# Optimization experiments

Measured on AMD Instinct MI355X. Metric: run time of the kernel, lower is better.

Reference implementation:

```python
import jax, jax.numpy as jnp
import numpy as np

B, C, H, W = 8, 64, 64, 64
PROJ = 8


def setup_inputs() -> dict:
    key = jax.random.key(0)
    ks = jax.random.split(key, 8)
    inp = {
        "query_x": jax.random.normal(ks[0], (B, C, H, W), dtype=jnp.float32),
        "ref_x": jax.random.normal(ks[1], (B, C, H, W), dtype=jnp.float32),
        # 1x1 conv weights stored as [out_ch, in_ch] (kernel_size=1)
        "wq": jax.random.normal(ks[2], (PROJ, C), dtype=jnp.float32) * 0.05,
        "bq": jnp.zeros((PROJ,), dtype=jnp.float32),
        "wk": jax.random.normal(ks[3], (PROJ, C), dtype=jnp.float32) * 0.05,
        "bk": jnp.zeros((PROJ,), dtype=jnp.float32),
        "wv": jax.random.normal(ks[4], (C, C), dtype=jnp.float32) * 0.05,
        "bv": jnp.zeros((C,), dtype=jnp.float32),
    }
    return inp


def reference(query_x, ref_x, wq, bq, wk, bk, wv, bv):
    b, c, h, w = ref_x.shape
    n = h * w
    # 1x1 conv projections, flattened to [B, ch, HW]
    q = (jnp.einsum("oc,bchw->bohw", wq, query_x) + bq[None, :, None, None]).reshape(b, PROJ, n)
    k = (jnp.einsum("oc,bchw->bohw", wk, ref_x) + bk[None, :, None, None]).reshape(b, PROJ, n)
    v = (jnp.einsum("oc,bchw->bohw", wv, ref_x) + bv[None, :, None, None]).reshape(b, c, n)
    # energy[b, j(ref), i(query)] = sum_p k[b,p,j] * q[b,p,i]  (unscaled)
    energy = jnp.einsum("bpj,bpi->bji", k, q)
    attention = jax.nn.softmax(energy, axis=-1)
    # z = bmm(v, attention^T): z[b,c,j] = sum_i v[b,c,i] * attention[b,j,i]
    z = jnp.einsum("bci,bji->bcj", v, attention).reshape(b, c, h, w)
    return query_x + z
```

## Files before the change

kernel.cpp:

```cpp
#include <hip/hip_runtime.h>
#include <hip/hip_bf16.h>

#define B_ 8
#define C_ 64
#define N_ 4096
#define ITERS 16

typedef __attribute__((ext_vector_type(4))) short bf16x4;
typedef __attribute__((ext_vector_type(8))) short bf16x8;
typedef __attribute__((ext_vector_type(4))) float f32x4;

static __device__ inline ushort f2bf(float x) {
    union { float f; unsigned u; } c; c.f = x;
    return (ushort)((c.u + 0x7FFFu + ((c.u >> 16) & 1u)) >> 16);
}
static __device__ inline short f2bfs(float x) {
    __hip_bfloat16 h = __float2bfloat16(x);
    return *reinterpret_cast<short*>(&h);
}
static __device__ inline int4 pack8(const ushort* s) {
    int4 r;
    r.x = (int)(s[0] | ((unsigned)s[1] << 16));
    r.y = (int)(s[2] | ((unsigned)s[3] << 16));
    r.z = (int)(s[4] | ((unsigned)s[5] << 16));
    r.w = (int)(s[6] | ((unsigned)s[7] << 16));
    return r;
}
static __device__ inline float exp2fast(float x) {
#if __has_builtin(__builtin_amdgcn_exp2f)
    return __builtin_amdgcn_exp2f(x);
#else
    return exp2f(x);
#endif
}

#if __has_builtin(__builtin_amdgcn_mfma_f32_16x16x16bf16_1k)
static __device__ inline f32x4 mfma16(bf16x4 a, bf16x4 b, f32x4 c) {
    return __builtin_amdgcn_mfma_f32_16x16x16bf16_1k(a, b, c, 0, 0, 0);
}
#else
static __device__ inline f32x4 mfma16(bf16x4 a, bf16x4 b, f32x4 c) {
    bf16x8 a8 = (bf16x8){a[0], a[1], a[2], a[3], 0, 0, 0, 0};
    bf16x8 b8 = (bf16x8){b[0], b[1], b[2], b[3], 0, 0, 0, 0};
    return __builtin_amdgcn_mfma_f32_16x16x32_bf16(a8, b8, c, 0, 0, 0);
}
#endif

static __device__ inline void gload16(const void* g, void* l) {
#if __has_builtin(__builtin_amdgcn_global_load_lds)
    __builtin_amdgcn_global_load_lds(
        (const __attribute__((address_space(1))) void*)g,
        (__attribute__((address_space(3))) void*)l, 16, 0, 0);
#else
    const int lane = threadIdx.x & 63;
    *(int4*)((char*)l + lane * 16) = *(const int4*)((const char*)g + lane * 16);
#endif
}

__global__ __launch_bounds__(256) void proj_kernel(
    const float* __restrict__ qx, const float* __restrict__ rx,
    const float* __restrict__ wq, const float* __restrict__ bq,
    const float* __restrict__ wk, const float* __restrict__ bk,
    const float* __restrict__ wv, const float* __restrict__ bv,
    ushort* __restrict__ qb, ushort* __restrict__ kb, ushort* __restrict__ vt2)
{
    const int og  = blockIdx.y;
    const int gid = blockIdx.x * 256 + threadIdx.x;
    const int b   = gid >> 12;
    const int i   = gid & (N_ - 1);

    if (og <= 1) {
        const float* xp = (og == 0 ? qx : rx) + (size_t)b * C_ * N_ + i;
        const float* wp = (og == 0 ? wq : wk);
        const float* bp = (og == 0 ? bq : bk);
        const float scale = (og == 0) ? 1.0f : 1.44269504088896340736f;
        float a[8];
#pragma unroll
        for (int p = 0; p < 8; ++p) a[p] = bp[p];
        for (int c = 0; c < C_; ++c) {
            const float x = xp[(size_t)c * N_];
#pragma unroll
            for (int p = 0; p < 8; ++p) a[p] = fmaf(wp[p * C_ + c], x, a[p]);
        }
        ushort u8[8];
#pragma unroll
        for (int p = 0; p < 8; ++p) u8[p] = f2bf(a[p] * scale);
        ushort* dst = (og == 0 ? qb : kb) + (size_t)gid * 8;
        *(int4*)dst = pack8(u8);
    } else {
        const int o0 = (og - 2) * 16;
        const float* xp = rx + (size_t)b * C_ * N_ + i;
        float a[16];
#pragma unroll
        for (int p = 0; p < 16; ++p) a[p] = bv[o0 + p];
        for (int c = 0; c < C_; ++c) {
            const float x = xp[(size_t)c * N_];
#pragma unroll
            for (int p = 0; p < 16; ++p)
                a[p] = fmaf(wv[(o0 + p) * C_ + c], x, a[p]);
        }
        const int t  = i >> 5;
        const int lo = i & 7;
        const int hi = (i >> 3) & 3;
        ushort* tb = vt2 + ((size_t)(b * 128 + t)) * 2048;
#pragma unroll
        for (int p = 0; p < 16; ++p) {
            const int c = o0 + p;
            tb[c * 32 + (((hi ^ ((c >> 1) & 3))) << 3) + lo] = f2bf(a[p]);
        }
    }
}

__global__ __launch_bounds__(512, 4) void attn_kernel(
    const ushort* __restrict__ qb, const ushort* __restrict__ kb,
    const ushort* __restrict__ vt2, const float* __restrict__ qx,
    float* __restrict__ out)
{
    __shared__ __align__(16) char smem[65536];
    float* o_lds    = (float*)smem;
    float* lsum_lds = (float*)(smem + 2 * 64 * 68 * 4);

    const int tid  = threadIdx.x;
    const int ig   = tid >> 6;
    const int lane = tid & 63;
    const int cc   = lane & 15;
    const int g    = lane >> 4;
    const int b    = blockIdx.y;
    const int j0   = blockIdx.x * 64;

    bf16x4 bk[4];
#pragma unroll
    for (int jb = 0; jb < 4; ++jb) bk[jb] = (bf16x4){0, 0, 0, 0};
    if (g < 2) {
#pragma unroll
        for (int jb = 0; jb < 4; ++jb)
            bk[jb] = *(const bf16x4*)(kb + ((size_t)b * N_ + j0 + jb * 16 + cc) * 8 + g * 4);
    }

    const int qperm = 8 * (cc >> 2) + (cc & 3);
    const ushort* qptr = qb + ((size_t)b * N_ + (size_t)ig * (N_ / 8) + qperm) * 8 + g * 4;

    const char* vsl = (const char*)vt2 + ((size_t)(b * 128 + ig * 16)) * 4096 + lane * 16;
    char* lds0 = smem + ig * 8192;

    f32x4 acc[4][4];
#pragma unroll
    for (int jb = 0; jb < 4; ++jb)
#pragma unroll
        for (int ct = 0; ct < 4; ++ct) acc[jb][ct] = (f32x4){0.f, 0.f, 0.f, 0.f};
    float ls[4] = {0.f, 0.f, 0.f, 0.f};
    const f32x4 zero4 = (f32x4){0.f, 0.f, 0.f, 0.f};

    {
        const char* s = vsl;
        char* d = lds0;
        gload16(s, d);
        gload16(s + 1024, d + 1024);
        gload16(s + 2048, d + 2048);
        gload16(s + 3072, d + 3072);
    }
    bf16x4 aq0 = *(const bf16x4*)(qptr);
    bf16x4 aq1 = *(const bf16x4*)(qptr + 32);

    const int rb = cc * 32 + ((g ^ ((cc >> 1) & 3)) << 3);

    int cur = 0;
#pragma unroll 1
    for (int it = 0; it < ITERS; ++it) {
        asm volatile("s_waitcnt vmcnt(0)" ::: "memory");
        __builtin_amdgcn_sched_barrier(0);

        const ushort* vtile = (const ushort*)(lds0 + cur * 4096);
        bf16x8 av0 = *(const bf16x8*)(vtile + rb);
        bf16x8 av1 = *(const bf16x8*)(vtile + rb + 512);
        bf16x8 av2 = *(const bf16x8*)(vtile + rb + 1024);
        bf16x8 av3 = *(const bf16x8*)(vtile + rb + 1536);

        const int nxt = (it + 1) & (ITERS - 1);
        {
            const char* s = vsl + (size_t)nxt * 4096;
            char* d = lds0 + (cur ^ 1) * 4096;
            gload16(s, d);
            gload16(s + 1024, d + 1024);
            gload16(s + 2048, d + 2048);
            gload16(s + 3072, d + 3072);
        }

#pragma unroll
        for (int jb = 0; jb < 4; ++jb) {
            f32x4 e0 = mfma16(aq0, bk[jb], zero4);
            f32x4 e1 = mfma16(aq1, bk[jb], zero4);
            float p[8];
#pragma unroll
            for (int r = 0; r < 4; ++r) {
                p[r]     = exp2fast(e0[r]);
                p[4 + r] = exp2fast(e1[r]);
            }
            bf16x8 pb;
#pragma unroll
            for (int e = 0; e < 8; ++e) pb[e] = f2bfs(p[e]);
            ls[jb] += ((p[0] + p[1]) + (p[2] + p[3])) +
                      ((p[4] + p[5]) + (p[6] + p[7]));
            acc[jb][0] = __builtin_amdgcn_mfma_f32_16x16x32_bf16(av0, pb, acc[jb][0], 0, 0, 0);
            acc[jb][1] = __builtin_amdgcn_mfma_f32_16x16x32_bf16(av1, pb, acc[jb][1], 0, 0, 0);
            acc[jb][2] = __builtin_amdgcn_mfma_f32_16x16x32_bf16(av2, pb, acc[jb][2], 0, 0, 0);
            acc[jb][3] = __builtin_amdgcn_mfma_f32_16x16x32_bf16(av3, pb, acc[jb][3], 0, 0, 0);
        }

        {
            const ushort* qp = qptr + (size_t)nxt * 256;
            aq0 = *(const bf16x4*)(qp);
            aq1 = *(const bf16x4*)(qp + 32);
        }
        cur ^= 1;
    }

#pragma unroll
    for (int jb = 0; jb < 4; ++jb) {
        ls[jb] += __shfl_xor(ls[jb], 16, 64);
        ls[jb] += __shfl_xor(ls[jb], 32, 64);
    }

    __syncthreads();
    {
        const int phme = ig >> 1;
        float* od = o_lds + (ig & 1) * (64 * 68);
        float* ld = lsum_lds + (ig & 1) * 64;
#pragma unroll 1
        for (int ph = 0; ph < 4; ++ph) {
            if (phme == ph) {
                if (ph == 0) {
#pragma unroll
                    for (int jb = 0; jb < 4; ++jb)
#pragma unroll
                        for (int ct = 0; ct < 4; ++ct)
#pragma unroll
                            for (int r = 0; r < 4; ++r)
                                od[(ct * 16 + 4 * g + r) * 68 + jb * 16 + cc] = acc[jb][ct][r];
                    if (g == 0) {
#pragma unroll
                        for (int jb = 0; jb < 4; ++jb) ld[jb * 16 + cc] = ls[jb];
                    }
                } else {
#pragma unroll
                    for (int jb = 0; jb < 4; ++jb)
#pragma unroll
                        for (int ct = 0; ct < 4; ++ct)
#pragma unroll
                            for (int r = 0; r < 4; ++r)
                                od[(ct * 16 + 4 * g + r) * 68 + jb * 16 + cc] += acc[jb][ct][r];
                    if (g == 0) {
#pragma unroll
                        for (int jb = 0; jb < 4; ++jb) ld[jb * 16 + cc] += ls[jb];
                    }
                }
            }
            __syncthreads();
        }
    }

    const int ec = tid >> 3;
    const int ej = (tid & 7) * 8;
    const float* xp = qx  + ((size_t)b * C_ + ec) * N_ + j0 + ej;
    float*       op = out + ((size_t)b * C_ + ec) * N_ + j0 + ej;
    float4 x0 = *(const float4*)xp;
    float4 x1 = *(const float4*)(xp + 4);
    float rr[8];
#pragma unroll
    for (int t = 0; t < 8; ++t) {
        const float num = o_lds[ec * 68 + ej + t] + o_lds[64 * 68 + ec * 68 + ej + t];
        const float den = lsum_lds[ej + t] + lsum_lds[64 + ej + t];
        rr[t] = num / den;
    }
    float4 r0 = make_float4(x0.x + rr[0], x0.y + rr[1], x0.z + rr[2], x0.w + rr[3]);
    float4 r1 = make_float4(x1.x + rr[4], x1.y + rr[5], x1.z + rr[6], x1.w + rr[7]);
    *(float4*)op       = r0;
    *(float4*)(op + 4) = r1;
}

extern "C" void kernel_launch(void* const* d_in, const int* in_sizes, int n_in,
                              void* d_out, int out_size, void* d_ws, size_t ws_size,
                              hipStream_t stream) {
    const float* qx = (const float*)d_in[0];
    const float* rx = (const float*)d_in[1];
    const float* wq = (const float*)d_in[2];
    const float* bq = (const float*)d_in[3];
    const float* wk = (const float*)d_in[4];
    const float* bk = (const float*)d_in[5];
    const float* wv = (const float*)d_in[6];
    const float* bv = (const float*)d_in[7];
    float* out = (float*)d_out;

    ushort* qb  = (ushort*)d_ws;
    ushort* kb  = qb + (size_t)B_ * N_ * 8;
    ushort* vt2 = kb + (size_t)B_ * N_ * 8;

    proj_kernel<<<dim3((B_ * N_) / 256, 6), 256, 0, stream>>>(
        qx, rx, wq, bq, wk, bk, wv, bv, qb, kb, vt2);

    attn_kernel<<<dim3(N_ / 64, B_), 512, 0, stream>>>(qb, kb, vt2, qx, out);
}
```

Measured before the change: 52.57 us.

## Fuse K/V projection reads, double-register Q prefetch, packed bf16 convert, swap grid order

The projection kernel drops from six to three output groups: one group computes K together with the first 32 V channels so ref_x is read fewer times, and each V group now covers 32 channels. The attention loop is unrolled by two with separate Q registers so Q loads are prefetched two iterations ahead, and it waits with vmcnt(2) instead of draining all loads. The exp results are converted with packed float2-to-bf16 intrinsics and summed as float2 vectors. The attention grid is transposed so batch is the fast block index. Larger per-thread accumulators (40 floats) raise register pressure in the projection kernel and halve its grid size.

```diff
diff --git a/kernel.cpp b/kernel.cpp
--- a/kernel.cpp
+++ b/kernel.cpp
@@ -8,23 +8,12 @@
 
 typedef __attribute__((ext_vector_type(4))) short bf16x4;
 typedef __attribute__((ext_vector_type(8))) short bf16x8;
+typedef __attribute__((ext_vector_type(2))) float f32x2;
 typedef __attribute__((ext_vector_type(4))) float f32x4;
 
 static __device__ inline ushort f2bf(float x) {
     union { float f; unsigned u; } c; c.f = x;
     return (ushort)((c.u + 0x7FFFu + ((c.u >> 16) & 1u)) >> 16);
-}
-static __device__ inline short f2bfs(float x) {
-    __hip_bfloat16 h = __float2bfloat16(x);
-    return *reinterpret_cast<short*>(&h);
-}
-static __device__ inline int4 pack8(const ushort* s) {
-    int4 r;
-    r.x = (int)(s[0] | ((unsigned)s[1] << 16));
-    r.y = (int)(s[2] | ((unsigned)s[3] << 16));
-    r.z = (int)(s[4] | ((unsigned)s[5] << 16));
-    r.w = (int)(s[6] | ((unsigned)s[7] << 16));
-    return r;
 }
 static __device__ inline float exp2fast(float x) {
 #if __has_builtin(__builtin_amdgcn_exp2f)
@@ -45,6 +34,9 @@
     return __builtin_amdgcn_mfma_f32_16x16x32_bf16(a8, b8, c, 0, 0, 0);
 }
 #endif
+static __device__ inline f32x4 mfma32(bf16x8 a, bf16x8 b, f32x4 c) {
+    return __builtin_amdgcn_mfma_f32_16x16x32_bf16(a, b, c, 0, 0, 0);
+}
 
 static __device__ inline void gload16(const void* g, void* l) {
 #if __has_builtin(__builtin_amdgcn_global_load_lds)
@@ -69,44 +61,72 @@
     const int b   = gid >> 12;
     const int i   = gid & (N_ - 1);
 
-    if (og <= 1) {
-        const float* xp = (og == 0 ? qx : rx) + (size_t)b * C_ * N_ + i;
-        const float* wp = (og == 0 ? wq : wk);
-        const float* bp = (og == 0 ? bq : bk);
-        const float scale = (og == 0) ? 1.0f : 1.44269504088896340736f;
+    const int t  = i >> 5;
+    const int lo = i & 7;
+    const int hi = (i >> 3) & 3;
+    ushort* tb = vt2 + ((size_t)(b * 128 + t)) * 2048;
+
+    if (og == 0) {
+        const float* xp = qx + (size_t)b * C_ * N_ + i;
         float a[8];
 #pragma unroll
-        for (int p = 0; p < 8; ++p) a[p] = bp[p];
+        for (int p = 0; p < 8; ++p) a[p] = bq[p];
         for (int c = 0; c < C_; ++c) {
             const float x = xp[(size_t)c * N_];
 #pragma unroll
-            for (int p = 0; p < 8; ++p) a[p] = fmaf(wp[p * C_ + c], x, a[p]);
+            for (int p = 0; p < 8; ++p) a[p] = fmaf(wq[p * C_ + c], x, a[p]);
         }
         ushort u8[8];
 #pragma unroll
-        for (int p = 0; p < 8; ++p) u8[p] = f2bf(a[p] * scale);
-        ushort* dst = (og == 0 ? qb : kb) + (size_t)gid * 8;
-        *(int4*)dst = pack8(u8);
-    } else {
-        const int o0 = (og - 2) * 16;
+        for (int p = 0; p < 8; ++p) u8[p] = f2bf(a[p]);
+        int4 r;
+        r.x = (int)(u8[0] | ((unsigned)u8[1] << 16));
+        r.y = (int)(u8[2] | ((unsigned)u8[3] << 16));
+        r.z = (int)(u8[4] | ((unsigned)u8[5] << 16));
+        r.w = (int)(u8[6] | ((unsigned)u8[7] << 16));
+        *(int4*)(qb + (size_t)gid * 8) = r;
+    } else if (og == 1) {
         const float* xp = rx + (size_t)b * C_ * N_ + i;
-        float a[16];
-#pragma unroll
-        for (int p = 0; p < 16; ++p) a[p] = bv[o0 + p];
+        float ak[8], av[32];
+#pragma unroll
+        for (int p = 0; p < 8; ++p) ak[p] = bk[p];
+#pragma unroll
+        for (int p = 0; p < 32; ++p) av[p] = bv[p];
         for (int c = 0; c < C_; ++c) {
             const float x = xp[(size_t)c * N_];
 #pragma unroll
-            for (int p = 0; p < 16; ++p)
-                a[p] = fmaf(wv[(o0 + p) * C_ + c], x, a[p]);
-        }
-        const int t  = i >> 5;
-        const int lo = i & 7;
-        const int hi = (i >> 3) & 3;
-        ushort* tb = vt2 + ((size_t)(b * 128 + t)) * 2048;
-#pragma unroll
-        for (int p = 0; p < 16; ++p) {
-            const int c = o0 + p;
-            tb[c * 32 + (((hi ^ ((c >> 1) & 3))) << 3) + lo] = f2bf(a[p]);
+            for (int p = 0; p < 8; ++p) ak[p] = fmaf(wk[p * C_ + c], x, ak[p]);
+#pragma unroll
+            for (int p = 0; p < 32; ++p) av[p] = fmaf(wv[p * C_ + c], x, av[p]);
+        }
+        const float s = 1.44269504088896340736f;
+        ushort u8[8];
+#pragma unroll
+        for (int p = 0; p < 8; ++p) u8[p] = f2bf(ak[p] * s);
+        int4 r;
+        r.x = (int)(u8[0] | ((unsigned)u8[1] << 16));
+        r.y = (int)(u8[2] | ((unsigned)u8[3] << 16));
+        r.z = (int)(u8[4] | ((unsigned)u8[5] << 16));
+        r.w = (int)(u8[6] | ((unsigned)u8[7] << 16));
+        *(int4*)(kb + (size_t)gid * 8) = r;
+#pragma unroll
+        for (int p = 0; p < 32; ++p)
+            tb[p * 32 + ((hi ^ ((p >> 1) & 3)) << 3) + lo] = f2bf(av[p]);
+    } else {
+        const float* xp = rx + (size_t)b * C_ * N_ + i;
+        float av[32];
+#pragma unroll
+        for (int p = 0; p < 32; ++p) av[p] = bv[32 + p];
+        for (int c = 0; c < C_; ++c) {
+            const float x = xp[(size_t)c * N_];
+#pragma unroll
+            for (int p = 0; p < 32; ++p)
+                av[p] = fmaf(wv[(32 + p) * C_ + c], x, av[p]);
+        }
+#pragma unroll
+        for (int p = 0; p < 32; ++p) {
+            const int c = 32 + p;
+            tb[c * 32 + ((hi ^ ((c >> 1) & 3)) << 3) + lo] = f2bf(av[p]);
         }
     }
 }
@@ -125,8 +145,8 @@
     const int lane = tid & 63;
     const int cc   = lane & 15;
     const int g    = lane >> 4;
-    const int b    = blockIdx.y;
-    const int j0   = blockIdx.x * 64;
+    const int b    = blockIdx.x;
+    const int j0   = blockIdx.y * 64;
 
     bf16x4 bk[4];
 #pragma unroll
@@ -148,75 +168,84 @@
     for (int jb = 0; jb < 4; ++jb)
 #pragma unroll
         for (int ct = 0; ct < 4; ++ct) acc[jb][ct] = (f32x4){0.f, 0.f, 0.f, 0.f};
-    float ls[4] = {0.f, 0.f, 0.f, 0.f};
+    f32x2 ls2[4];
+#pragma unroll
+    for (int jb = 0; jb < 4; ++jb) ls2[jb] = (f32x2){0.f, 0.f};
     const f32x4 zero4 = (f32x4){0.f, 0.f, 0.f, 0.f};
 
-    {
-        const char* s = vsl;
-        char* d = lds0;
-        gload16(s, d);
-        gload16(s + 1024, d + 1024);
-        gload16(s + 2048, d + 2048);
-        gload16(s + 3072, d + 3072);
-    }
-    bf16x4 aq0 = *(const bf16x4*)(qptr);
-    bf16x4 aq1 = *(const bf16x4*)(qptr + 32);
-
     const int rb = cc * 32 + ((g ^ ((cc >> 1) & 3)) << 3);
 
-    int cur = 0;
+    bf16x4 qa0 = *(const bf16x4*)(qptr);
+    bf16x4 qa1 = *(const bf16x4*)(qptr + 32);
+    gload16(vsl, lds0);
+    gload16(vsl + 1024, lds0 + 1024);
+    gload16(vsl + 2048, lds0 + 2048);
+    gload16(vsl + 3072, lds0 + 3072);
+    bf16x4 qb0 = *(const bf16x4*)(qptr + 256);
+    bf16x4 qb1 = *(const bf16x4*)(qptr + 256 + 32);
+    asm volatile("s_waitcnt vmcnt(0)" ::: "memory");
+    __builtin_amdgcn_sched_barrier(0);
+
+#define HALF_ITER(Q0, Q1, RBOFF, WBOFF, IT)                                    \
+    {                                                                          \
+        asm volatile("s_waitcnt vmcnt(2)" ::: "memory");                       \
+        __builtin_amdgcn_sched_barrier(0);                                     \
+        const ushort* vtile = (const ushort*)(lds0 + (RBOFF));                 \
+        bf16x8 av0 = *(const bf16x8*)(vtile + rb);                             \
+        bf16x8 av1 = *(const bf16x8*)(vtile + rb + 512);                       \
+        bf16x8 av2 = *(const bf16x8*)(vtile + rb + 1024);                      \
+        bf16x8 av3 = *(const bf16x8*)(vtile + rb + 1536);                      \
+        {                                                                      \
+            const int nxt = ((IT) + 1) & (ITERS - 1);                          \
+            const char* s = vsl + (size_t)nxt * 4096;                          \
+            char* dd = lds0 + (WBOFF);                                         \
+            gload16(s, dd);                                                    \
+            gload16(s + 1024, dd + 1024);                                      \
+            gload16(s + 2048, dd + 2048);                                      \
+            gload16(s + 3072, dd + 3072);                                      \
+        }                                                                      \
+        __builtin_amdgcn_sched_barrier(0);                                     \
+        _Pragma("unroll")                                                      \
+        for (int jb = 0; jb < 4; ++jb) {                                       \
+            f32x4 e0 = mfma16(Q0, bk[jb], zero4);                              \
+            f32x4 e1 = mfma16(Q1, bk[jb], zero4);                              \
+            float p0 = exp2fast(e0[0]), p1 = exp2fast(e0[1]);                  \
+            float p2 = exp2fast(e0[2]), p3 = exp2fast(e0[3]);                  \
+            float p4 = exp2fast(e1[0]), p5 = exp2fast(e1[1]);                  \
+            float p6 = exp2fast(e1[2]), p7 = exp2fast(e1[3]);                  \
+            union { bf16x8 v; __hip_bfloat162 h[4]; } pu;                      \
+            pu.h[0] = __float22bfloat162_rn(make_float2(p0, p1));              \
+            pu.h[1] = __float22bfloat162_rn(make_float2(p2, p3));              \
+            pu.h[2] = __float22bfloat162_rn(make_float2(p4, p5));              \
+            pu.h[3] = __float22bfloat162_rn(make_float2(p6, p7));              \
+            f32x2 sA = (f32x2){p0, p1} + (f32x2){p2, p3};                      \
+            f32x2 sB = (f32x2){p4, p5} + (f32x2){p6, p7};                      \
+            ls2[jb] += sA + sB;                                                \
+            acc[jb][0] = mfma32(av0, pu.v, acc[jb][0]);                        \
+            acc[jb][1] = mfma32(av1, pu.v, acc[jb][1]);                        \
+            acc[jb][2] = mfma32(av2, pu.v, acc[jb][2]);                        \
+            acc[jb][3] = mfma32(av3, pu.v, acc[jb][3]);                        \
+        }                                                                      \
+        {                                                                      \
+            const int nq = ((IT) + 2) & (ITERS - 1);                           \
+            const ushort* qp = qptr + (size_t)nq * 256;                        \
+            Q0 = *(const bf16x4*)(qp);                                         \
+            Q1 = *(const bf16x4*)(qp + 32);                                    \
+        }                                                                      \
+    }
+
 #pragma unroll 1
-    for (int it = 0; it < ITERS; ++it) {
-        asm volatile("s_waitcnt vmcnt(0)" ::: "memory");
-        __builtin_amdgcn_sched_barrier(0);
-
-        const ushort* vtile = (const ushort*)(lds0 + cur * 4096);
-        bf16x8 av0 = *(const bf16x8*)(vtile + rb);
-        bf16x8 av1 = *(const bf16x8*)(vtile + rb + 512);
-        bf16x8 av2 = *(const bf16x8*)(vtile + rb + 1024);
-        bf16x8 av3 = *(const bf16x8*)(vtile + rb + 1536);
-
-        const int nxt = (it + 1) & (ITERS - 1);
-        {
-            const char* s = vsl + (size_t)nxt * 4096;
-            char* d = lds0 + (cur ^ 1) * 4096;
-            gload16(s, d);
-            gload16(s + 1024, d + 1024);
-            gload16(s + 2048, d + 2048);
-            gload16(s + 3072, d + 3072);
-        }
-
-#pragma unroll
-        for (int jb = 0; jb < 4; ++jb) {
-            f32x4 e0 = mfma16(aq0, bk[jb], zero4);
-            f32x4 e1 = mfma16(aq1, bk[jb], zero4);
-            float p[8];
-#pragma unroll
-            for (int r = 0; r < 4; ++r) {
-                p[r]     = exp2fast(e0[r]);
-                p[4 + r] = exp2fast(e1[r]);
-            }
-            bf16x8 pb;
-#pragma unroll
-            for (int e = 0; e < 8; ++e) pb[e] = f2bfs(p[e]);
-            ls[jb] += ((p[0] + p[1]) + (p[2] + p[3])) +
-                      ((p[4] + p[5]) + (p[6] + p[7]));
-            acc[jb][0] = __builtin_amdgcn_mfma_f32_16x16x32_bf16(av0, pb, acc[jb][0], 0, 0, 0);
-            acc[jb][1] = __builtin_amdgcn_mfma_f32_16x16x32_bf16(av1, pb, acc[jb][1], 0, 0, 0);
-            acc[jb][2] = __builtin_amdgcn_mfma_f32_16x16x32_bf16(av2, pb, acc[jb][2], 0, 0, 0);
-            acc[jb][3] = __builtin_amdgcn_mfma_f32_16x16x32_bf16(av3, pb, acc[jb][3], 0, 0, 0);
-        }
-
-        {
-            const ushort* qp = qptr + (size_t)nxt * 256;
-            aq0 = *(const bf16x4*)(qp);
-            aq1 = *(const bf16x4*)(qp + 32);
-        }
-        cur ^= 1;
-    }
-
+    for (int d = 0; d < ITERS / 2; ++d) {
+        const int it0 = 2 * d;
+        HALF_ITER(qa0, qa1, 0, 4096, it0);
+        HALF_ITER(qb0, qb1, 4096, 0, it0 + 1);
+    }
+#undef HALF_ITER
+
+    float ls[4];
 #pragma unroll
     for (int jb = 0; jb < 4; ++jb) {
+        ls[jb] = ls2[jb][0] + ls2[jb][1];
         ls[jb] += __shfl_xor(ls[jb], 16, 64);
         ls[jb] += __shfl_xor(ls[jb], 32, 64);
     }
@@ -295,8 +324,8 @@
     ushort* kb  = qb + (size_t)B_ * N_ * 8;
     ushort* vt2 = kb + (size_t)B_ * N_ * 8;
 
-    proj_kernel<<<dim3((B_ * N_) / 256, 6), 256, 0, stream>>>(
+    proj_kernel<<<dim3((B_ * N_) / 256, 3), 256, 0, stream>>>(
         qx, rx, wq, bq, wk, bk, wv, bv, qb, kb, vt2);
 
-    attn_kernel<<<dim3(N_ / 64, B_), 512, 0, stream>>>(qb, kb, vt2, qx, out);
-}
+    attn_kernel<<<dim3(B_, N_ / 64), 512, 0, stream>>>(qb, kb, vt2, qx, out);
+}
```

Result: no change. 52.57 us (-0.0%).
